# Kernel optimization log

Measured on AMD Instinct MI355X. Metric: run time of the kernel, lower is better.

## Reference

```python
import jax, jax.numpy as jnp
import numpy as np

B, C_FEAT, H_F, W_F = 16, 256, 80, 80
C_ILL, K, H_Z, W_Z = 64, 3, 40, 40


def setup_inputs() -> dict:
    key = jax.random.key(0)
    k1, k2, k3, k4, k5, k6, k7 = jax.random.split(key, 7)
    feat = jax.random.normal(k1, (B, C_FEAT, H_F, W_F), dtype=jnp.float32)
    Z = jax.random.normal(k2, (B, C_ILL, H_Z, W_Z), dtype=jnp.float32)
    P = jax.random.uniform(k3, (B, K, H_Z, W_Z), dtype=jnp.float32)
    # Expert 1x1-conv params (original zero-inits; use small random for nontrivial math)
    Wg = jax.random.normal(k4, (K, C_FEAT, C_ILL), dtype=jnp.float32) * 0.02
    bg = jax.random.normal(k5, (K, C_FEAT), dtype=jnp.float32) * 0.02
    Wb = jax.random.normal(k6, (K, C_FEAT, C_ILL), dtype=jnp.float32) * 0.02
    bb = jax.random.normal(k7, (K, C_FEAT), dtype=jnp.float32) * 0.02
    return {"feat": feat, "Z": Z, "P": P, "Wg": Wg, "bg": bg, "Wb": Wb, "bb": bb}


def reference(feat, Z, P, Wg, bg, Wb, bb):
    Bb, C, H, W = feat.shape
    # bilinear upsample, half-pixel centers (== torch align_corners=False)
    Z_up = jax.image.resize(Z, (Z.shape[0], Z.shape[1], H, W), method='bilinear')
    P_up = jax.image.resize(P, (P.shape[0], P.shape[1], H, W), method='bilinear')
    # router-weighted illumination features: [B,K,D,H,W]
    ZP = jnp.einsum('bkhw,bdhw->bkdhw', P_up, Z_up)
    # soft-routed 1x1-conv experts, fused across K (weights + router-weighted biases)
    delta_gamma = jnp.einsum('bkdhw,kcd->bchw', ZP, Wg) + jnp.einsum('bkhw,kc->bchw', P_up, bg)
    delta_beta = jnp.einsum('bkdhw,kcd->bchw', ZP, Wb) + jnp.einsum('bkhw,kc->bchw', P_up, bb)
    # FiLM residual modulation
    return feat * (1.0 + delta_gamma) + delta_beta
```

## Files before the change

kernel.cpp:

```cpp
#include <hip/hip_runtime.h>
#include <hip/hip_bf16.h>

#define NB   16
#define NC   256
#define HF   80
#define WF   80
#define NPIX 6400
#define ND   64
#define NK   3
#define NKC  7
#define NPB  400
#define A_G_STRIDE  (NKC * 4 * 512)


typedef __bf16 bf16;
typedef __bf16 bf16x8 __attribute__((ext_vector_type(8)));
typedef float  floatx4 __attribute__((ext_vector_type(4)));

#define GLOBAL_AS __attribute__((address_space(1)))
#define LDS_AS    __attribute__((address_space(3)))

__global__ __launch_bounds__(256) void prep_kernel(
    const float* __restrict__ Z, const float* __restrict__ P,
    const float* __restrict__ Wg, const float* __restrict__ bg,
    const float* __restrict__ Wb, const float* __restrict__ bb,
    float* __restrict__ ZF, float* __restrict__ PU, bf16* __restrict__ A2)
{
    __shared__ float z_up[WF][ND + 1];
    __shared__ float p_up[WF][NK];

    const int bid = blockIdx.x;
    const int t   = threadIdx.x;

    if (bid >= NB * HF) {
        int i = (bid - NB * HF) * 256 + t;
        int lane = i & 63;
        int j2 = i >> 6;
        int mt = j2 & 3;
        int j3 = j2 >> 2;
        int kc = j3 % 7;
        int g  = j3 / 7;
        int l15 = lane & 15, q = lane >> 4;
        int cbase = (g >> 1) * 64 + (g & 1) * 32;
        int c = cbase + (mt & 1) * 16 + l15;
        const float* W    = (mt >= 2) ? Wb : Wg;
        const float* bias = (mt >= 2) ? bb : bg;
        int kd0 = kc * 32 + q * 8;

        bf16x8 v;
        if (kd0 < NK * ND) {
            int k = kd0 >> 6, d = kd0 & 63;
            const float* src = W + ((size_t)k * NC + c) * ND + d;
            #pragma unroll
            for (int j = 0; j < 8; ++j) v[j] = (bf16)src[j];
        } else if (kd0 == NK * ND) {
            #pragma unroll
            for (int j = 0; j < 8; ++j) v[j] = (bf16)0.0f;
            v[0] = (bf16)bias[0 * NC + c];
            v[1] = (bf16)bias[1 * NC + c];
            v[2] = (bf16)bias[2 * NC + c];
        } else {
            #pragma unroll
            for (int j = 0; j < 8; ++j) v[j] = (bf16)0.0f;
        }
        *reinterpret_cast<bf16x8*>(A2 + (size_t)i * 8) = v;
        return;
    }

    const int b   = bid / HF;
    const int h   = bid - b * HF;

    float srch = 0.5f * (float)h - 0.25f;
    float flh  = floorf(srch);
    float fh   = srch - flh;
    int h0 = (int)flh, h1 = h0 + 1;
    h0 = max(h0, 0); h1 = min(h1, 40 - 1);

    #pragma unroll 4
    for (int i = 0; i < 20; ++i) {
        int e = t + 256 * i;
        int d = e / WF;
        int w = e - d * WF;
        float srcw = 0.5f * (float)w - 0.25f;
        float flw  = floorf(srcw);
        float fw   = srcw - flw;
        int w0 = (int)flw, w1 = w0 + 1;
        w0 = max(w0, 0); w1 = min(w1, 40 - 1);
        const float* Zr = Z + (size_t)(b * ND + d) * (40 * 40);
        float z00 = Zr[h0 * 40 + w0], z01 = Zr[h0 * 40 + w1];
        float z10 = Zr[h1 * 40 + w0], z11 = Zr[h1 * 40 + w1];
        float zi0 = z00 + fw * (z01 - z00);
        float zi1 = z10 + fw * (z11 - z10);
        z_up[w][d] = zi0 + fh * (zi1 - zi0);
    }
    if (t < WF * NK) {
        int w = t / NK;
        int k = t - w * NK;
        float srcw = 0.5f * (float)w - 0.25f;
        float flw  = floorf(srcw);
        float fw   = srcw - flw;
        int w0 = (int)flw, w1 = w0 + 1;
        w0 = max(w0, 0); w1 = min(w1, 40 - 1);
        const float* Pr = P + (size_t)(b * NK + k) * (40 * 40);
        float p00 = Pr[h0 * 40 + w0], p01 = Pr[h0 * 40 + w1];
        float p10 = Pr[h1 * 40 + w0], p11 = Pr[h1 * 40 + w1];
        float pi0 = p00 + fw * (p01 - p00);
        float pi1 = p10 + fw * (p11 - p10);
        p_up[w][k] = pi0 + fh * (pi1 - pi0);
    }
    __syncthreads();

    for (int i = t; i < 640; i += 256) {
        int lane = i & 63;
        int j2   = i >> 6;
        int half = j2 & 1;
        int pb_l = j2 >> 1;
        int l15 = lane & 15, q = lane >> 4;
        int w   = pb_l * 16 + l15;
        int d0  = half * 32 + q * 8;
        float* dst = ZF + ((((size_t)(b * NPB + h * 5 + pb_l)) * 2 + half) * 64 + lane) * 8;
        floatx4 v0, v1;
        #pragma unroll
        for (int j = 0; j < 4; ++j) { v0[j] = z_up[w][d0 + j]; v1[j] = z_up[w][d0 + 4 + j]; }
        *reinterpret_cast<floatx4*>(dst)     = v0;
        *reinterpret_cast<floatx4*>(dst + 4) = v1;
    }
    if (t < 240) {
        int pb_l = t / 48;
        int rem  = t - pb_l * 48;
        int k    = rem >> 4;
        int l15  = rem & 15;
        PU[(((size_t)(b * NPB + h * 5 + pb_l)) * 3 + k) * 16 + l15] = p_up[pb_l * 16 + l15][k];
    }
}

__global__ __launch_bounds__(256) void gemm_film_kernel(
    const bf16* __restrict__ A2, const float* __restrict__ ZF,
    const float* __restrict__ PU,
    const float* __restrict__ feat, float* __restrict__ out)
{
    __shared__ __attribute__((aligned(16))) bf16 Alds[28 * 512];

    const int ntb = blockIdx.x;
    const int b   = blockIdx.y;
    const int g   = blockIdx.z;
    const int tid  = threadIdx.x;
    const int lane = tid & 63;
    const int nh   = tid >> 6;
    const int l15  = lane & 15;
    const int q    = lane >> 4;

    const int cbase = (g >> 1) * 64 + (g & 1) * 32;
    const int pb0   = ntb * 8 + nh * 2;
    const int pix0  = pb0 * 16;

    {
        const bf16* gA = A2 + (size_t)g * A_G_STRIDE;
        #pragma unroll
        for (int j7 = 0; j7 < 7; ++j7) {
            int j = nh * 7 + j7;
            __builtin_amdgcn_global_load_lds(
                (const GLOBAL_AS void*)(gA + (size_t)j * 512 + lane * 8),
                (LDS_AS void*)(&Alds[j * 512]), 16, 0, 0);
        }
    }

    floatx4 zf[2][2][2];
    #pragma unroll
    for (int nt = 0; nt < 2; ++nt)
        #pragma unroll
        for (int hf = 0; hf < 2; ++hf) {
            const float* cp = ZF + ((((size_t)(b * NPB + pb0 + nt)) * 2 + hf) * 64 + lane) * 8;
            zf[nt][hf][0] = *reinterpret_cast<const floatx4*>(cp);
            zf[nt][hf][1] = *reinterpret_cast<const floatx4*>(cp + 4);
        }
    float pv[2][3];
    #pragma unroll
    for (int nt = 0; nt < 2; ++nt)
        #pragma unroll
        for (int k = 0; k < 3; ++k)
            pv[nt][k] = PU[(((size_t)(b * NPB + pb0 + nt)) * 3 + k) * 16 + l15];

    const float* featb = feat + ((size_t)(b * NC + cbase + l15)) * NPIX + pix0 + q * 4;
    floatx4 fv[2][2];
    #pragma unroll
    for (int mt = 0; mt < 2; ++mt)
        #pragma unroll
        for (int nt = 0; nt < 2; ++nt)
            fv[mt][nt] = *reinterpret_cast<const floatx4*>(
                featb + (size_t)mt * 16 * NPIX + nt * 16);

    __syncthreads();

    floatx4 acc[4][2] = {};

    #pragma unroll
    for (int kc = 0; kc < NKC; ++kc) {
        bf16x8 af[4];
        #pragma unroll
        for (int mt = 0; mt < 4; ++mt)
            af[mt] = *reinterpret_cast<const bf16x8*>(
                &Alds[(kc * 4 + mt) * 512 + lane * 8]);

        bf16x8 bfr[2];
        if (kc < 6) {
            const int hf = kc & 1;
            const int k  = kc >> 1;
            #pragma unroll
            for (int nt = 0; nt < 2; ++nt) {
                float p = pv[nt][k];
                #pragma unroll
                for (int j = 0; j < 4; ++j) {
                    bfr[nt][j]     = (bf16)(p * zf[nt][hf][0][j]);
                    bfr[nt][j + 4] = (bf16)(p * zf[nt][hf][1][j]);
                }
            }
        } else {
            #pragma unroll
            for (int nt = 0; nt < 2; ++nt) {
                #pragma unroll
                for (int j = 0; j < 8; ++j) bfr[nt][j] = (bf16)0.0f;
                if (q == 0) {
                    bfr[nt][0] = (bf16)pv[nt][0];
                    bfr[nt][1] = (bf16)pv[nt][1];
                    bfr[nt][2] = (bf16)pv[nt][2];
                }
            }
        }
        #pragma unroll
        for (int mt = 0; mt < 4; ++mt)
            #pragma unroll
            for (int nt = 0; nt < 2; ++nt)
                acc[mt][nt] = __builtin_amdgcn_mfma_f32_16x16x32_bf16(
                    bfr[nt], af[mt], acc[mt][nt], 0, 0, 0);
    }

    float* outb = out + ((size_t)(b * NC + cbase + l15)) * NPIX + pix0 + q * 4;
    #pragma unroll
    for (int mt = 0; mt < 2; ++mt) {
        #pragma unroll
        for (int nt = 0; nt < 2; ++nt) {
            floatx4 f  = fv[mt][nt];
            floatx4 ga = acc[mt][nt];
            floatx4 be = acc[mt + 2][nt];
            floatx4 o;
            #pragma unroll
            for (int j = 0; j < 4; ++j)
                o[j] = f[j] * (1.0f + ga[j]) + be[j];
            *reinterpret_cast<floatx4*>(outb + (size_t)mt * 16 * NPIX + nt * 16) = o;
        }
    }
}

extern "C" void kernel_launch(void* const* d_in, const int* in_sizes, int n_in,
                              void* d_out, int out_size, void* d_ws, size_t ws_size,
                              hipStream_t stream)
{
    (void)in_sizes; (void)n_in; (void)out_size; (void)ws_size;
    const float* feat = (const float*)d_in[0];
    const float* Z    = (const float*)d_in[1];
    const float* P    = (const float*)d_in[2];
    const float* Wg   = (const float*)d_in[3];
    const float* bg   = (const float*)d_in[4];
    const float* Wb   = (const float*)d_in[5];
    const float* bb   = (const float*)d_in[6];

    float* ZF = (float*)d_ws;
    float* PU = ZF + (size_t)NB * NPB * 2 * 64 * 8;
    bf16*  Apk = (bf16*)(PU + (size_t)NB * NPB * 3 * 16);
    float* out = (float*)d_out;

    prep_kernel<<<NB * HF + 56, 256, 0, stream>>>(Z, P, Wg, bg, Wb, bb, ZF, PU, Apk);

    dim3 grid(NPIX / 128, NB, 8);
    gemm_film_kernel<<<grid, 256, 0, stream>>>(Apk, ZF, PU, feat, out);
}
```

Before: 238.1 us.

## Make GEMM-FiLM kernel persistent over 8 tiles with double-buffered Z/P prefetch

The grid shrinks from 6400 blocks to 800, and each block now loops over 8 consecutive (batch, pixel-tile) units. The A weight slice is staged into LDS once per block and reused across those 8 tiles instead of being reloaded per tile. Z/P operands for the next tile are prefetched into a second register buffer while the current tile computes. The trade-off is higher register pressure and fewer resident waves, so there is less parallelism to hide the latency of the feat loads and output stores, which are still issued per tile.

```diff
diff --git a/kernel.cpp b/kernel.cpp
--- a/kernel.cpp
+++ b/kernel.cpp
@@ -141,18 +141,14 @@
 {
     __shared__ __attribute__((aligned(16))) bf16 Alds[28 * 512];
 
-    const int ntb = blockIdx.x;
-    const int b   = blockIdx.y;
-    const int g   = blockIdx.z;
+    const int slot = blockIdx.x;
+    const int g    = blockIdx.y;
     const int tid  = threadIdx.x;
     const int lane = tid & 63;
     const int nh   = tid >> 6;
     const int l15  = lane & 15;
     const int q    = lane >> 4;
-
     const int cbase = (g >> 1) * 64 + (g & 1) * 32;
-    const int pb0   = ntb * 8 + nh * 2;
-    const int pix0  = pb0 * 16;
 
     {
         const bf16* gA = A2 + (size_t)g * A_G_STRIDE;
@@ -165,91 +161,116 @@
         }
     }
 
-    floatx4 zf[2][2][2];
+    floatx4 zfb[2][2][2][2];
+    float   pvb[2][2][3];
+
+#define ISSUE(s, tau_)                                                         \
+    {                                                                          \
+        const int tb_  = (tau_) / 50;                                          \
+        const int ntb_ = (tau_) - tb_ * 50;                                     \
+        const int pb_  = ntb_ * 8 + nh * 2;                                     \
+        _Pragma("unroll")                                                      \
+        for (int nt_ = 0; nt_ < 2; ++nt_) {                                     \
+            _Pragma("unroll")                                                  \
+            for (int hf_ = 0; hf_ < 2; ++hf_) {                                 \
+                const float* cp_ = ZF +                                         \
+                    ((((size_t)(tb_ * NPB + pb_ + nt_)) * 2 + hf_) * 64 + lane) * 8; \
+                zfb[s][nt_][hf_][0] = *reinterpret_cast<const floatx4*>(cp_);   \
+                zfb[s][nt_][hf_][1] = *reinterpret_cast<const floatx4*>(cp_ + 4);\
+            }                                                                  \
+            _Pragma("unroll")                                                  \
+            for (int k_ = 0; k_ < 3; ++k_)                                      \
+                pvb[s][nt_][k_] =                                               \
+                    PU[(((size_t)(tb_ * NPB + pb_ + nt_)) * 3 + k_) * 16 + l15];\
+        }                                                                      \
+    }
+
+    ISSUE(0, slot * 8);
+    __syncthreads();
+
     #pragma unroll
-    for (int nt = 0; nt < 2; ++nt)
-        #pragma unroll
-        for (int hf = 0; hf < 2; ++hf) {
-            const float* cp = ZF + ((((size_t)(b * NPB + pb0 + nt)) * 2 + hf) * 64 + lane) * 8;
-            zf[nt][hf][0] = *reinterpret_cast<const floatx4*>(cp);
-            zf[nt][hf][1] = *reinterpret_cast<const floatx4*>(cp + 4);
-        }
-    float pv[2][3];
-    #pragma unroll
-    for (int nt = 0; nt < 2; ++nt)
-        #pragma unroll
-        for (int k = 0; k < 3; ++k)
-            pv[nt][k] = PU[(((size_t)(b * NPB + pb0 + nt)) * 3 + k) * 16 + l15];
-
-    const float* featb = feat + ((size_t)(b * NC + cbase + l15)) * NPIX + pix0 + q * 4;
-    floatx4 fv[2][2];
-    #pragma unroll
-    for (int mt = 0; mt < 2; ++mt)
-        #pragma unroll
-        for (int nt = 0; nt < 2; ++nt)
-            fv[mt][nt] = *reinterpret_cast<const floatx4*>(
-                featb + (size_t)mt * 16 * NPIX + nt * 16);
-
-    __syncthreads();
-
-    floatx4 acc[4][2] = {};
-
-    #pragma unroll
-    for (int kc = 0; kc < NKC; ++kc) {
-        bf16x8 af[4];
-        #pragma unroll
-        for (int mt = 0; mt < 4; ++mt)
-            af[mt] = *reinterpret_cast<const bf16x8*>(
-                &Alds[(kc * 4 + mt) * 512 + lane * 8]);
-
-        bf16x8 bfr[2];
-        if (kc < 6) {
-            const int hf = kc & 1;
-            const int k  = kc >> 1;
-            #pragma unroll
-            for (int nt = 0; nt < 2; ++nt) {
-                float p = pv[nt][k];
-                #pragma unroll
-                for (int j = 0; j < 4; ++j) {
-                    bfr[nt][j]     = (bf16)(p * zf[nt][hf][0][j]);
-                    bfr[nt][j + 4] = (bf16)(p * zf[nt][hf][1][j]);
+    for (int i = 0; i < 8; ++i) {
+        const int cur = i & 1;
+        const int nxt = cur ^ 1;
+        const int tau = slot * 8 + i;
+        const int tb  = tau / 50;
+        const int ntb = tau - tb * 50;
+        const int pb0 = ntb * 8 + nh * 2;
+        const int pix0 = pb0 * 16;
+
+        const float* featb = feat + ((size_t)(tb * NC + cbase + l15)) * NPIX
+                             + pix0 + q * 4;
+        floatx4 fv[2][2];
+        #pragma unroll
+        for (int mt = 0; mt < 2; ++mt)
+            #pragma unroll
+            for (int nt = 0; nt < 2; ++nt)
+                fv[mt][nt] = *reinterpret_cast<const floatx4*>(
+                    featb + (size_t)mt * 16 * NPIX + nt * 16);
+
+        if (i < 7) ISSUE(nxt, tau + 1);
+
+        floatx4 acc[4][2] = {};
+
+        #pragma unroll
+        for (int kc = 0; kc < NKC; ++kc) {
+            bf16x8 af[4];
+            #pragma unroll
+            for (int mt = 0; mt < 4; ++mt)
+                af[mt] = *reinterpret_cast<const bf16x8*>(
+                    &Alds[(kc * 4 + mt) * 512 + lane * 8]);
+
+            bf16x8 bfr[2];
+            if (kc < 6) {
+                const int hf = kc & 1;
+                const int k  = kc >> 1;
+                #pragma unroll
+                for (int nt = 0; nt < 2; ++nt) {
+                    float p = pvb[cur][nt][k];
+                    #pragma unroll
+                    for (int j = 0; j < 4; ++j) {
+                        bfr[nt][j]     = (bf16)(p * zfb[cur][nt][hf][0][j]);
+                        bfr[nt][j + 4] = (bf16)(p * zfb[cur][nt][hf][1][j]);
+                    }
+                }
+            } else {
+                #pragma unroll
+                for (int nt = 0; nt < 2; ++nt) {
+                    #pragma unroll
+                    for (int j = 0; j < 8; ++j) bfr[nt][j] = (bf16)0.0f;
+                    if (q == 0) {
+                        bfr[nt][0] = (bf16)pvb[cur][nt][0];
+                        bfr[nt][1] = (bf16)pvb[cur][nt][1];
+                        bfr[nt][2] = (bf16)pvb[cur][nt][2];
+                    }
                 }
             }
-        } else {
+            #pragma unroll
+            for (int mt = 0; mt < 4; ++mt)
+                #pragma unroll
+                for (int nt = 0; nt < 2; ++nt)
+                    acc[mt][nt] = __builtin_amdgcn_mfma_f32_16x16x32_bf16(
+                        bfr[nt], af[mt], acc[mt][nt], 0, 0, 0);
+        }
+
+        float* outb = out + ((size_t)(tb * NC + cbase + l15)) * NPIX
+                      + pix0 + q * 4;
+        #pragma unroll
+        for (int mt = 0; mt < 2; ++mt) {
             #pragma unroll
             for (int nt = 0; nt < 2; ++nt) {
-                #pragma unroll
-                for (int j = 0; j < 8; ++j) bfr[nt][j] = (bf16)0.0f;
-                if (q == 0) {
-                    bfr[nt][0] = (bf16)pv[nt][0];
-                    bfr[nt][1] = (bf16)pv[nt][1];
-                    bfr[nt][2] = (bf16)pv[nt][2];
-                }
+                floatx4 f  = fv[mt][nt];
+                floatx4 ga = acc[mt][nt];
+                floatx4 be = acc[mt + 2][nt];
+                floatx4 o;
+                #pragma unroll
+                for (int j = 0; j < 4; ++j)
+                    o[j] = f[j] * (1.0f + ga[j]) + be[j];
+                *reinterpret_cast<floatx4*>(outb + (size_t)mt * 16 * NPIX + nt * 16) = o;
             }
         }
-        #pragma unroll
-        for (int mt = 0; mt < 4; ++mt)
-            #pragma unroll
-            for (int nt = 0; nt < 2; ++nt)
-                acc[mt][nt] = __builtin_amdgcn_mfma_f32_16x16x32_bf16(
-                    bfr[nt], af[mt], acc[mt][nt], 0, 0, 0);
-    }
-
-    float* outb = out + ((size_t)(b * NC + cbase + l15)) * NPIX + pix0 + q * 4;
-    #pragma unroll
-    for (int mt = 0; mt < 2; ++mt) {
-        #pragma unroll
-        for (int nt = 0; nt < 2; ++nt) {
-            floatx4 f  = fv[mt][nt];
-            floatx4 ga = acc[mt][nt];
-            floatx4 be = acc[mt + 2][nt];
-            floatx4 o;
-            #pragma unroll
-            for (int j = 0; j < 4; ++j)
-                o[j] = f[j] * (1.0f + ga[j]) + be[j];
-            *reinterpret_cast<floatx4*>(outb + (size_t)mt * 16 * NPIX + nt * 16) = o;
-        }
-    }
+    }
+#undef ISSUE
 }
 
 extern "C" void kernel_launch(void* const* d_in, const int* in_sizes, int n_in,
@@ -272,6 +293,6 @@
 
     prep_kernel<<<NB * HF + 56, 256, 0, stream>>>(Z, P, Wg, bg, Wb, bb, ZF, PU, Apk);
 
-    dim3 grid(NPIX / 128, NB, 8);
+    dim3 grid(100, 8, 1);
     gemm_film_kernel<<<grid, 256, 0, stream>>>(Apk, ZF, PU, feat, out);
 }
```

Measured after the change: 248.9 us. 1.05x slower.
